# Performance work log

Measured on AMD Instinct MI355X. Metric: run time of the kernel, lower is better.

Reference implementation:

```python
import jax, jax.numpy as jnp
import numpy as np

NUM_GROUPS = 32
EPS = 1e-6


def group_norm(x, gamma, beta):
    # x: [B, C, H, W]
    B, C, H, W = x.shape
    xg = x.reshape(B, NUM_GROUPS, C // NUM_GROUPS, H, W)
    mean = jnp.mean(xg, axis=(2, 3, 4), keepdims=True)
    var = jnp.var(xg, axis=(2, 3, 4), keepdims=True)
    xn = (xg - mean) * jax.lax.rsqrt(var + EPS)
    xn = xn.reshape(B, C, H, W)
    return xn * gamma[None, :, None, None] + beta[None, :, None, None]


def conv1x1(x, w, b):
    # x: [B, C, H, W], w: [Cout, Cin], b: [Cout]
    return jnp.einsum('bchw,dc->bdhw', x, w) + b[None, :, None, None]


def setup_inputs() -> dict:
    key = jax.random.key(0)
    ks = jax.random.split(key, 11)
    B, C, H, W = 4, 512, 64, 64
    s = 1.0 / np.sqrt(C)
    return {
        'x': jax.random.normal(ks[0], (B, C, H, W), dtype=jnp.float32),
        'gn_gamma': jnp.ones((C,), dtype=jnp.float32),
        'gn_beta': jnp.zeros((C,), dtype=jnp.float32),
        'wq': jax.random.normal(ks[1], (C, C), dtype=jnp.float32) * s,
        'bq': jax.random.normal(ks[2], (C,), dtype=jnp.float32) * 0.01,
        'wk': jax.random.normal(ks[3], (C, C), dtype=jnp.float32) * s,
        'bk': jax.random.normal(ks[4], (C,), dtype=jnp.float32) * 0.01,
        'wv': jax.random.normal(ks[5], (C, C), dtype=jnp.float32) * s,
        'bv': jax.random.normal(ks[6], (C,), dtype=jnp.float32) * 0.01,
        'wo': jax.random.normal(ks[7], (C, C), dtype=jnp.float32) * s,
        'bo': jax.random.normal(ks[8], (C,), dtype=jnp.float32) * 0.01,
    }


def reference(x, gn_gamma, gn_beta, wq, bq, wk, bk, wv, bv, wo, bo):
    B, C, H, W = x.shape
    h = group_norm(x, gn_gamma, gn_beta)
    q = conv1x1(h, wq, bq).reshape(B, C, H * W)  # [B, C, N]
    k = conv1x1(h, wk, bk).reshape(B, C, H * W)
    v = conv1x1(h, wv, bv).reshape(B, C, H * W)
    scale = jnp.asarray(C, x.dtype) ** -0.5
    # scores[b, i, j] = q_i . k_j
    scores = jnp.einsum('bci,bcj->bij', q, k) * scale  # [B, N, N]
    attn = jax.nn.softmax(scores, axis=2)
    # out[b, c, i] = sum_j v[b, c, j] * attn[b, i, j]
    out = jnp.einsum('bcj,bij->bci', v, attn).reshape(B, C, H, W)
    out = conv1x1(out, wo, bo)
    return x + out
```

## Files before the change

### kernel.cpp

```cpp
#include <hip/hip_runtime.h>

using uint = unsigned int;
typedef short bf16x8 __attribute__((ext_vector_type(8)));
typedef _Float16 f16x8 __attribute__((ext_vector_type(8)));
typedef float f32x4 __attribute__((ext_vector_type(4)));
typedef long i64;
typedef i64 i64x2 __attribute__((ext_vector_type(2)));
typedef i64 i64x4 __attribute__((ext_vector_type(4)));
typedef int i32x8 __attribute__((ext_vector_type(8)));
typedef unsigned short u16x4 __attribute__((ext_vector_type(4)));

static constexpr int Cc = 512;
static constexpr int Nn = 4096;
static constexpr size_t NC = (size_t)Nn * Cc;
static constexpr size_t SN = (size_t)Nn * Nn;

__device__ __forceinline__ unsigned short f2bf(float f) {
    unsigned int u = __builtin_bit_cast(unsigned int, f);
    u = (u + 0x7fff + ((u >> 16) & 1)) >> 16;
    return (unsigned short)u;
}
__device__ __forceinline__ unsigned short f2h(float f) {
    _Float16 h = (_Float16)f;
    return __builtin_bit_cast(unsigned short, h);
}

__device__ __forceinline__ int sig64(int j) {
    return (j & ~63) | (((j >> 2) & 3) << 4) | (((j >> 4) & 3) << 2) | (j & 3);
}

__device__ __forceinline__ void gll16(const void* g, void* l) {
    __builtin_amdgcn_global_load_lds(
        (const __attribute__((address_space(1))) void*)g,
        (__attribute__((address_space(3))) void*)l, 16, 0, 0);
}

__device__ __forceinline__ f32x4 mfma_fp8_k128(i32x8 a, i32x8 b, f32x4 c) {
    return __builtin_amdgcn_mfma_scale_f32_16x16x128_f8f6f4(
        a, b, c, 0 , 0 , 0, 0x7F7F7F7F, 0, 0x7F7F7F7F);
}

__device__ __forceinline__ i32x8 ld_frag256(const unsigned char* base, int R, int g0) {
    const unsigned char* p = base + R * 128;
    i64x2 l0 = *(const i64x2*)(p + ((g0 ^ (R & 7)) << 4));
    i64x2 l1 = *(const i64x2*)(p + (((g0 + 1) ^ (R & 7)) << 4));
    i64x4 c4 = {l0[0], l0[1], l1[0], l1[1]};
    return __builtin_bit_cast(i32x8, c4);
}

__global__ void cvt4_kernel(const float* __restrict__ wa, const float* __restrict__ wb,
                            const float* __restrict__ wc, const float* __restrict__ wd,
                            unsigned short* __restrict__ out) {
    const float* ins[4] = {wa, wb, wc, wd};
    const float* in = ins[blockIdx.y];
    unsigned short* o = out + (size_t)blockIdx.y * 262144;
    int i = blockIdx.x * blockDim.x + threadIdx.x;
    float4 v = ((const float4*)in)[i];
    o[i * 4 + 0] = f2bf(v.x);
    o[i * 4 + 1] = f2bf(v.y);
    o[i * 4 + 2] = f2bf(v.z);
    o[i * 4 + 3] = f2bf(v.w);
}

__global__ void gn_stats_kernel(const float* __restrict__ x, float* __restrict__ meanb,
                                float* __restrict__ rsb) {
    int bg = blockIdx.x;
    const float* slab = x + (size_t)bg * 16 * Nn;
    const float4* s4 = (const float4*)slab;
    int t = threadIdx.x;
    float s1 = 0.f, s2 = 0.f;
#pragma unroll 8
    for (int k = 0; k < 64; ++k) {
        float4 v = s4[k * 256 + t];
        s1 += v.x + v.y + v.z + v.w;
        s2 += v.x * v.x + v.y * v.y + v.z * v.z + v.w * v.w;
    }
#pragma unroll
    for (int o = 32; o > 0; o >>= 1) { s1 += __shfl_down(s1, o); s2 += __shfl_down(s2, o); }
    __shared__ float r1[4], r2[4];
    int wv_ = t >> 6, ln = t & 63;
    if (ln == 0) { r1[wv_] = s1; r2[wv_] = s2; }
    __syncthreads();
    if (t == 0) {
        float a1 = r1[0] + r1[1] + r1[2] + r1[3];
        float a2 = r2[0] + r2[1] + r2[2] + r2[3];
        float mean = a1 * (1.f / 65536.f);
        float var = a2 * (1.f / 65536.f) - mean * mean;
        meanb[bg] = mean;
        rsb[bg] = rsqrtf(var + 1e-6f);
    }
}

__global__ __launch_bounds__(256) void gn_norm_kernel(
    const float* __restrict__ x, const float* __restrict__ meanb, const float* __restrict__ rsb,
    const float* __restrict__ gamma, const float* __restrict__ beta,
    unsigned short* __restrict__ h_t) {
    __shared__ float tile[64][65];
    int n0 = blockIdx.x * 64, c0 = blockIdx.y * 64, b = blockIdx.z;
    int t = threadIdx.x;
    const float* xb = x + (size_t)b * Cc * Nn;
#pragma unroll
    for (int j = 0; j < 4; ++j) {
        int i = j * 256 + t;
        int c = i >> 4;
        int n4 = i & 15;
        int cg = c0 + c;
        float4 v = ((const float4*)(xb + (size_t)cg * Nn + n0))[n4];
        int g = cg >> 4;
        float mean = meanb[b * 32 + g], rs = rsb[b * 32 + g];
        float ga = gamma[cg] * rs;
        float be = beta[cg] - mean * ga;
        tile[n4 * 4 + 0][c] = v.x * ga + be;
        tile[n4 * 4 + 1][c] = v.y * ga + be;
        tile[n4 * 4 + 2][c] = v.z * ga + be;
        tile[n4 * 4 + 3][c] = v.w * ga + be;
    }
    __syncthreads();
    int n = t >> 2;
    int cpart = (t & 3) * 16;
    unsigned short o[16];
#pragma unroll
    for (int q = 0; q < 16; ++q) o[q] = f2bf(tile[n][cpart + q]);
    unsigned short* dst = h_t + (size_t)b * NC + (size_t)(n0 + n) * Cc + c0 + cpart;
    ((uint4*)dst)[0] = ((uint4*)o)[0];
    ((uint4*)dst)[1] = ((uint4*)o)[1];
}

template <int BM, int DT, int BIAS_MODE, int OUT_MODE, int HAS_RES>
__global__ __launch_bounds__(256, 2) void gemm_bt(
    const unsigned short* __restrict__ A, int lda, size_t sA,
    const unsigned short* __restrict__ Bt, int ldb, size_t sB,
    void* __restrict__ outp, int ldc, size_t sC,
    const float* __restrict__ bias,
    const float* __restrict__ res, size_t sR,
    int K, float alpha,
    const float* __restrict__ bias2, void* __restrict__ outp2, int nsplit) {
    constexpr int MT = BM / 32;
    __shared__ unsigned short lA[BM * 64];
    __shared__ unsigned short lB[128 * 64];
    int z = blockIdx.z;
    A += (size_t)z * sA;
    Bt += (size_t)z * sB;
    int m0 = blockIdx.y * BM, n0 = blockIdx.x * 128;
    int ncol0 = n0;
    if (nsplit && n0 >= nsplit) { bias = bias2; outp = outp2; ncol0 = n0 - nsplit; }
    int t = threadIdx.x;
    int lane = t & 63, wave = t >> 6;
    int wm = wave >> 1, wn = wave & 1;
    int lo = lane & 15, quad = lane >> 4;

    f32x4 acc[MT][4];
#pragma unroll
    for (int a1 = 0; a1 < MT; ++a1)
#pragma unroll
        for (int a2 = 0; a2 < 4; ++a2) acc[a1][a2] = (f32x4){0.f, 0.f, 0.f, 0.f};

    for (int k0 = 0; k0 < K; k0 += 64) {
#pragma unroll
        for (int p = 0; p < MT; ++p) {
            int ci = p * 256 + t;
            int row = ci >> 3;
            int gs = (ci ^ row) & 7;
            gll16(A + (size_t)(m0 + row) * lda + k0 + gs * 8, &lA[(size_t)ci * 8]);
        }
#pragma unroll
        for (int p = 0; p < 4; ++p) {
            int ci = p * 256 + t;
            int row = ci >> 3;
            int gs = (ci ^ row) & 7;
            gll16(Bt + (size_t)(n0 + row) * ldb + k0 + gs * 8, &lB[(size_t)ci * 8]);
        }
        __syncthreads();
#pragma unroll
        for (int ks = 0; ks < 2; ++ks) {
            int G = quad + ks * 4;
            bf16x8 af[MT], bfr[4];
#pragma unroll
            for (int mt = 0; mt < MT; ++mt) {
                int R = wm * (BM / 2) + mt * 16 + lo;
                af[mt] = *(const bf16x8*)&lA[R * 64 + (((G ^ R) & 7) << 3)];
            }
#pragma unroll
            for (int nt = 0; nt < 4; ++nt) {
                int R = wn * 64 + nt * 16 + lo;
                bfr[nt] = *(const bf16x8*)&lB[R * 64 + (((G ^ R) & 7) << 3)];
            }
#pragma unroll
            for (int mt = 0; mt < MT; ++mt)
#pragma unroll
                for (int nt = 0; nt < 4; ++nt) {
                    if (DT == 0)
                        acc[mt][nt] = __builtin_amdgcn_mfma_f32_16x16x32_bf16(af[mt], bfr[nt], acc[mt][nt], 0, 0, 0);
                    else
                        acc[mt][nt] = __builtin_amdgcn_mfma_f32_16x16x32_f16(
                            __builtin_bit_cast(f16x8, af[mt]), __builtin_bit_cast(f16x8, bfr[nt]),
                            acc[mt][nt], 0, 0, 0);
                }
        }
        __syncthreads();
    }

    size_t zc = (size_t)z * sC;
    float* outf = (float*)outp + zc;
    unsigned short* outb = (unsigned short*)outp + zc;
    unsigned char* outc = (unsigned char*)outp + zc;
    const float* resz = HAS_RES ? res + (size_t)z * sR : nullptr;

#pragma unroll
    for (int mt = 0; mt < MT; ++mt) {
#pragma unroll
        for (int nt = 0; nt < 4; ++nt) {
            int row = m0 + wm * (BM / 2) + mt * 16 + quad * 4;
            int col = ncol0 + wn * 64 + nt * 16 + lo;
            float bn = (BIAS_MODE == 2) ? bias[col] : 0.f;
#pragma unroll
            for (int r = 0; r < 4; ++r) {
                float vv = acc[mt][nt][r];
                if (BIAS_MODE == 1) vv += bias[row + r];
                if (BIAS_MODE == 2) vv += bn;
                vv *= alpha;
                if (OUT_MODE == 3 || OUT_MODE == 4) {
                    float e = fmaxf(fminf(vv, 448.f), -448.f);
                    int pk = __builtin_amdgcn_cvt_pk_fp8_f32(e, e, 0, false);
                    int cp = (OUT_MODE == 4) ? sig64(col) : col;
                    outc[(size_t)(row + r) * ldc + cp] = (unsigned char)(pk & 0xff);
                } else {
                    size_t off = (size_t)(row + r) * ldc + col;
                    if (HAS_RES) vv += resz[off];
                    if (OUT_MODE == 0) outf[off] = vv;
                    else if (OUT_MODE == 1) outb[off] = f2bf(vv);
                    else outb[off] = f2h(vv);
                }
            }
        }
    }
}

__global__ __launch_bounds__(256, 3) void qk_fp8(
    const unsigned char* __restrict__ Q, const unsigned char* __restrict__ Kt,
    unsigned char* __restrict__ S, float alpha) {
    __shared__ unsigned char lA[128 * 128];
    __shared__ unsigned char lB[128 * 128];
    int z = blockIdx.z;
    Q += (size_t)z * NC;
    Kt += (size_t)z * NC;
    S += (size_t)z * SN;
    int m0 = blockIdx.y * 128, n0 = blockIdx.x * 128;
    int t = threadIdx.x;
    int lane = t & 63, wave = t >> 6;
    int wm = wave >> 1, wn = wave & 1;
    int lo = lane & 15, quad = lane >> 4;

    f32x4 acc[4][4];
#pragma unroll
    for (int a1 = 0; a1 < 4; ++a1)
#pragma unroll
        for (int a2 = 0; a2 < 4; ++a2) acc[a1][a2] = (f32x4){0.f, 0.f, 0.f, 0.f};

    for (int k0 = 0; k0 < Cc; k0 += 128) {
#pragma unroll
        for (int p = 0; p < 4; ++p) {
            int ci = p * 256 + t;
            int row = ci >> 3, g = ci & 7;
            int gs = g ^ (row & 7);
            gll16(Q + (size_t)(m0 + row) * Cc + k0 + gs * 16, &lA[ci * 16]);
        }
#pragma unroll
        for (int p = 0; p < 4; ++p) {
            int ci = p * 256 + t;
            int row = ci >> 3, g = ci & 7;
            int gs = g ^ (row & 7);
            gll16(Kt + (size_t)(n0 + row) * Cc + k0 + gs * 16, &lB[ci * 16]);
        }
        __syncthreads();
        int g0 = quad * 2;
        i32x8 qf[4];
#pragma unroll
        for (int qt = 0; qt < 4; ++qt) qf[qt] = ld_frag256(lA, wm * 64 + qt * 16 + lo, g0);
#pragma unroll
        for (int jt = 0; jt < 4; ++jt) {
            i32x8 kf = ld_frag256(lB, wn * 64 + jt * 16 + lo, g0);
#pragma unroll
            for (int qt = 0; qt < 4; ++qt)
                acc[jt][qt] = mfma_fp8_k128(kf, qf[qt], acc[jt][qt]);
        }
        __syncthreads();
    }

    const float L2E = 1.4426950408889634f;
    float a2 = alpha * L2E;
    float b2 = -2.f * L2E;
#pragma unroll
    for (int qt = 0; qt < 4; ++qt) {
        int q = m0 + wm * 64 + qt * 16 + lo;
        uint w[4];
#pragma unroll
        for (int jt = 0; jt < 4; ++jt) {
            float e0 = fminf(exp2f(fmaf(acc[jt][qt][0], a2, b2)), 448.f);
            float e1 = fminf(exp2f(fmaf(acc[jt][qt][1], a2, b2)), 448.f);
            float e2 = fminf(exp2f(fmaf(acc[jt][qt][2], a2, b2)), 448.f);
            float e3 = fminf(exp2f(fmaf(acc[jt][qt][3], a2, b2)), 448.f);
            int d = __builtin_amdgcn_cvt_pk_fp8_f32(e0, e1, 0, false);
            d = __builtin_amdgcn_cvt_pk_fp8_f32(e2, e3, d, true);
            w[jt] = (uint)d;
        }
        *(uint4*)&S[(size_t)q * Nn + n0 + wn * 64 + quad * 16] =
            make_uint4(w[0], w[1], w[2], w[3]);
    }
}

__global__ __launch_bounds__(256, 3) void pv_fp8(
    const unsigned char* __restrict__ S, const unsigned char* __restrict__ V,
    unsigned short* __restrict__ o_t) {
    __shared__ unsigned char lA[128 * 128];
    __shared__ unsigned char lB[128 * 128];
    int z = blockIdx.z;
    S += (size_t)z * SN;
    V += (size_t)z * NC;
    o_t += (size_t)z * NC;
    int m0 = blockIdx.y * 128, n0 = blockIdx.x * 128;
    int t = threadIdx.x;
    int lane = t & 63, wave = t >> 6;
    int wm = wave >> 1, wn = wave & 1;
    int lo = lane & 15, quad = lane >> 4;

    f32x4 acc[4][4];
    f32x4 rs[4];
#pragma unroll
    for (int a1 = 0; a1 < 4; ++a1) {
        rs[a1] = (f32x4){0.f, 0.f, 0.f, 0.f};
#pragma unroll
        for (int a2 = 0; a2 < 4; ++a2) acc[a1][a2] = (f32x4){0.f, 0.f, 0.f, 0.f};
    }
    const int OB = 0x38383838;
    const i32x8 ones = {OB, OB, OB, OB, OB, OB, OB, OB};

    for (int k0 = 0; k0 < Nn; k0 += 128) {
#pragma unroll
        for (int p = 0; p < 4; ++p) {
            int ci = p * 256 + t;
            int row = ci >> 3, g = ci & 7;
            int gs = g ^ (row & 7);
            gll16(S + (size_t)(m0 + row) * Nn + k0 + gs * 16, &lA[ci * 16]);
        }
#pragma unroll
        for (int p = 0; p < 4; ++p) {
            int ci = p * 256 + t;
            int row = ci >> 3, g = ci & 7;
            int gs = g ^ (row & 7);
            gll16(V + (size_t)(n0 + row) * Nn + k0 + gs * 16, &lB[ci * 16]);
        }
        __syncthreads();
        int g0 = quad * 2;
        i32x8 sf[4];
#pragma unroll
        for (int qt = 0; qt < 4; ++qt) {
            sf[qt] = ld_frag256(lA, wm * 64 + qt * 16 + lo, g0);
            rs[qt] = mfma_fp8_k128(ones, sf[qt], rs[qt]);
        }
#pragma unroll
        for (int ct = 0; ct < 4; ++ct) {
            i32x8 vf = ld_frag256(lB, wn * 64 + ct * 16 + lo, g0);
#pragma unroll
            for (int qt = 0; qt < 4; ++qt)
                acc[ct][qt] = mfma_fp8_k128(vf, sf[qt], acc[ct][qt]);
        }
        __syncthreads();
    }

#pragma unroll
    for (int qt = 0; qt < 4; ++qt) {
        int q = m0 + wm * 64 + qt * 16 + lo;
        float inv = 1.f / rs[qt][0];
#pragma unroll
        for (int ct = 0; ct < 4; ++ct) {
            int c = n0 + wn * 64 + ct * 16 + quad * 4;
            u16x4 o;
            o[0] = f2bf(acc[ct][qt][0] * inv);
            o[1] = f2bf(acc[ct][qt][1] * inv);
            o[2] = f2bf(acc[ct][qt][2] * inv);
            o[3] = f2bf(acc[ct][qt][3] * inv);
            *(u16x4*)&o_t[(size_t)q * Cc + c] = o;
        }
    }
}

extern "C" void kernel_launch(void* const* d_in, const int* in_sizes, int n_in,
                              void* d_out, int out_size, void* d_ws, size_t ws_size,
                              hipStream_t stream) {
    const float* x     = (const float*)d_in[0];
    const float* gamma = (const float*)d_in[1];
    const float* beta  = (const float*)d_in[2];
    const float* wq = (const float*)d_in[3];
    const float* bq = (const float*)d_in[4];
    const float* wk = (const float*)d_in[5];
    const float* bk = (const float*)d_in[6];
    const float* wv = (const float*)d_in[7];
    const float* bv = (const float*)d_in[8];
    const float* wo = (const float*)d_in[9];
    const float* bo = (const float*)d_in[10];

    char* ws = (char*)d_ws;
    unsigned short* h_t  = (unsigned short*)(ws);
    unsigned char*  q_8  = (unsigned char*)(ws + 16777216);
    unsigned char*  k_8  = (unsigned char*)(ws + 33554432);
    unsigned char*  v_8  = (unsigned char*)(ws + 50331648);
    unsigned short* o_t  = (unsigned short*)(ws + 67108864);
    unsigned char*  S    = (unsigned char*)(ws + 83886080);
    unsigned short* wqb  = (unsigned short*)(ws + 218103808);
    unsigned short* wvb  = (unsigned short*)(ws + 219152384);
    unsigned short* wob  = (unsigned short*)(ws + 219676672);
    float* statm         = (float*)(ws + 220200960);
    float* statr         = (float*)(ws + 220201984);

    const float SCALE = 0.044194173824159216f;

    cvt4_kernel<<<dim3(256, 4), 256, 0, stream>>>(wq, wk, wv, wo, wqb);

    gn_stats_kernel<<<128, 256, 0, stream>>>(x, statm, statr);
    gn_norm_kernel<<<dim3(64, 8, 4), 256, 0, stream>>>(x, statm, statr, gamma, beta, h_t);

    gemm_bt<128, 0, 2, 3, 0><<<dim3(8, 32, 4), 256, 0, stream>>>(
        h_t, Cc, NC, wqb, Cc, 0, q_8, Cc, NC, bq, nullptr, 0, Cc, 1.f, bk, k_8, 512);
    gemm_bt<128, 0, 1, 4, 0><<<dim3(32, 4, 4), 256, 0, stream>>>(
        wvb, Cc, 0, h_t, Cc, NC, v_8, Nn, NC, bv, nullptr, 0, Cc, 1.f, nullptr, nullptr, 0);

    qk_fp8<<<dim3(32, 32, 4), 256, 0, stream>>>(q_8, k_8, S, SCALE);
    pv_fp8<<<dim3(4, 32, 4), 256, 0, stream>>>(S, v_8, o_t);

    gemm_bt<128, 0, 1, 0, 1><<<dim3(32, 4, 4), 256, 0, stream>>>(
        wob, Cc, 0, o_t, Cc, NC, d_out, Nn, NC, bo, x, NC, Cc, 1.f, nullptr, nullptr, 0);
}
```

Baseline: 282.9 us.

## Split GN stats across more blocks with atomics, add MFMA priority, permute output layout

Group-norm statistics are split eight ways per group with atomic accumulation of sums, and mean/rstd are computed in the normalize kernel; a zero kernel clears the accumulators first. The QK and PV loops raise wave priority around the MFMA sections. The PV epilogue writes 16 contiguous bf16 values per lane with two 16-byte stores, and the wo weight is converted into a permuted column order so the output projection reads it consistently. The aim is more parallelism for the stats pass and wider stores, at the cost of an extra launch and atomic float summation order.

New measurement: 286.8 us. About the same (+1.4%).

```diff
diff --git a/kernel.cpp b/kernel.cpp
--- a/kernel.cpp
+++ b/kernel.cpp
@@ -48,6 +48,11 @@
     return __builtin_bit_cast(i32x8, c4);
 }
 
+__global__ void zero_kernel(float* __restrict__ p, int n4) {
+    int i = blockIdx.x * blockDim.x + threadIdx.x;
+    if (i < n4) ((float4*)p)[i] = make_float4(0.f, 0.f, 0.f, 0.f);
+}
+
 __global__ void cvt4_kernel(const float* __restrict__ wa, const float* __restrict__ wb,
                             const float* __restrict__ wc, const float* __restrict__ wd,
                             unsigned short* __restrict__ out) {
@@ -56,21 +61,30 @@
     unsigned short* o = out + (size_t)blockIdx.y * 262144;
     int i = blockIdx.x * blockDim.x + threadIdx.x;
     float4 v = ((const float4*)in)[i];
-    o[i * 4 + 0] = f2bf(v.x);
-    o[i * 4 + 1] = f2bf(v.y);
-    o[i * 4 + 2] = f2bf(v.z);
-    o[i * 4 + 3] = f2bf(v.w);
-}
-
-__global__ void gn_stats_kernel(const float* __restrict__ x, float* __restrict__ meanb,
-                                float* __restrict__ rsb) {
-    int bg = blockIdx.x;
-    const float* slab = x + (size_t)bg * 16 * Nn;
-    const float4* s4 = (const float4*)slab;
+    int e = i * 4;
+    int idx;
+    if (blockIdx.y == 3) {
+        int m = e >> 9, k = e & 511;
+        int kp = (k & ~63) | (((k >> 2) & 3) << 4) | (((k >> 4) & 3) << 2);
+        idx = m * 512 + kp;
+    } else {
+        idx = e;
+    }
+    o[idx + 0] = f2bf(v.x);
+    o[idx + 1] = f2bf(v.y);
+    o[idx + 2] = f2bf(v.z);
+    o[idx + 3] = f2bf(v.w);
+}
+
+__global__ void gn_stats_kernel(const float* __restrict__ x, float* __restrict__ sums,
+                                float* __restrict__ sqs) {
+    int bid = blockIdx.x;
+    int bg = bid >> 3, sub = bid & 7;
+    const float4* s4 = (const float4*)(x + (size_t)bg * 65536) + sub * 2048;
     int t = threadIdx.x;
     float s1 = 0.f, s2 = 0.f;
-#pragma unroll 8
-    for (int k = 0; k < 64; ++k) {
+#pragma unroll
+    for (int k = 0; k < 8; ++k) {
         float4 v = s4[k * 256 + t];
         s1 += v.x + v.y + v.z + v.w;
         s2 += v.x * v.x + v.y * v.y + v.z * v.z + v.w * v.w;
@@ -82,17 +96,13 @@
     if (ln == 0) { r1[wv_] = s1; r2[wv_] = s2; }
     __syncthreads();
     if (t == 0) {
-        float a1 = r1[0] + r1[1] + r1[2] + r1[3];
-        float a2 = r2[0] + r2[1] + r2[2] + r2[3];
-        float mean = a1 * (1.f / 65536.f);
-        float var = a2 * (1.f / 65536.f) - mean * mean;
-        meanb[bg] = mean;
-        rsb[bg] = rsqrtf(var + 1e-6f);
+        atomicAdd(&sums[bg], r1[0] + r1[1] + r1[2] + r1[3]);
+        atomicAdd(&sqs[bg], r2[0] + r2[1] + r2[2] + r2[3]);
     }
 }
 
 __global__ __launch_bounds__(256) void gn_norm_kernel(
-    const float* __restrict__ x, const float* __restrict__ meanb, const float* __restrict__ rsb,
+    const float* __restrict__ x, const float* __restrict__ sums, const float* __restrict__ sqs,
     const float* __restrict__ gamma, const float* __restrict__ beta,
     unsigned short* __restrict__ h_t) {
     __shared__ float tile[64][65];
@@ -107,7 +117,10 @@
         int cg = c0 + c;
         float4 v = ((const float4*)(xb + (size_t)cg * Nn + n0))[n4];
         int g = cg >> 4;
-        float mean = meanb[b * 32 + g], rs = rsb[b * 32 + g];
+        float sm = sums[b * 32 + g], sq = sqs[b * 32 + g];
+        float mean = sm * (1.f / 65536.f);
+        float var = sq * (1.f / 65536.f) - mean * mean;
+        float rs = rsqrtf(var + 1e-6f);
         float ga = gamma[cg] * rs;
         float be = beta[cg] - mean * ga;
         tile[n4 * 4 + 0][c] = v.x * ga + be;
@@ -277,6 +290,7 @@
         i32x8 qf[4];
 #pragma unroll
         for (int qt = 0; qt < 4; ++qt) qf[qt] = ld_frag256(lA, wm * 64 + qt * 16 + lo, g0);
+        __builtin_amdgcn_s_setprio(1);
 #pragma unroll
         for (int jt = 0; jt < 4; ++jt) {
             i32x8 kf = ld_frag256(lB, wn * 64 + jt * 16 + lo, g0);
@@ -284,6 +298,7 @@
             for (int qt = 0; qt < 4; ++qt)
                 acc[jt][qt] = mfma_fp8_k128(kf, qf[qt], acc[jt][qt]);
         }
+        __builtin_amdgcn_s_setprio(0);
         __syncthreads();
     }
 
@@ -353,6 +368,7 @@
         __syncthreads();
         int g0 = quad * 2;
         i32x8 sf[4];
+        __builtin_amdgcn_s_setprio(1);
 #pragma unroll
         for (int qt = 0; qt < 4; ++qt) {
             sf[qt] = ld_frag256(lA, wm * 64 + qt * 16 + lo, g0);
@@ -365,6 +381,7 @@
             for (int qt = 0; qt < 4; ++qt)
                 acc[ct][qt] = mfma_fp8_k128(vf, sf[qt], acc[ct][qt]);
         }
+        __builtin_amdgcn_s_setprio(0);
         __syncthreads();
     }
 
@@ -372,16 +389,15 @@
     for (int qt = 0; qt < 4; ++qt) {
         int q = m0 + wm * 64 + qt * 16 + lo;
         float inv = 1.f / rs[qt][0];
-#pragma unroll
-        for (int ct = 0; ct < 4; ++ct) {
-            int c = n0 + wn * 64 + ct * 16 + quad * 4;
-            u16x4 o;
-            o[0] = f2bf(acc[ct][qt][0] * inv);
-            o[1] = f2bf(acc[ct][qt][1] * inv);
-            o[2] = f2bf(acc[ct][qt][2] * inv);
-            o[3] = f2bf(acc[ct][qt][3] * inv);
-            *(u16x4*)&o_t[(size_t)q * Cc + c] = o;
-        }
+        unsigned short o16[16];
+#pragma unroll
+        for (int ct = 0; ct < 4; ++ct)
+#pragma unroll
+            for (int r = 0; r < 4; ++r)
+                o16[ct * 4 + r] = f2bf(acc[ct][qt][r] * inv);
+        unsigned short* dst = &o_t[(size_t)q * Cc + n0 + wn * 64 + quad * 16];
+        ((uint4*)dst)[0] = ((uint4*)o16)[0];
+        ((uint4*)dst)[1] = ((uint4*)o16)[1];
     }
 }
 
@@ -415,9 +431,11 @@
 
     const float SCALE = 0.044194173824159216f;
 
+    zero_kernel<<<1, 128, 0, stream>>>(statm, 128);
+
     cvt4_kernel<<<dim3(256, 4), 256, 0, stream>>>(wq, wk, wv, wo, wqb);
 
-    gn_stats_kernel<<<128, 256, 0, stream>>>(x, statm, statr);
+    gn_stats_kernel<<<1024, 256, 0, stream>>>(x, statm, statr);
     gn_norm_kernel<<<dim3(64, 8, 4), 256, 0, stream>>>(x, statm, statr, gamma, beta, h_t);
 
     gemm_bt<128, 0, 2, 3, 0><<<dim3(8, 32, 4), 256, 0, stream>>>(
```
